# Performance work log

Hardware: AMD Instinct MI355X
Metric: run time of the kernel (lower is better)

Reference implementation:

```python
import jax, jax.numpy as jnp
import numpy as np

G = 128          # occupancy/feature grid resolution (hardcoded in module)
S = 128          # marching steps per ray (max_steps)
N_RAYS = 262144  # 512x512 image
AABB_MIN = jnp.array([-1.0, -0.5, -1.0], dtype=jnp.float32)
AABB_MAX = jnp.array([ 1.0,  0.5,  1.0], dtype=jnp.float32)
MIN_NEAR = 0.05
DENSITY_THRESH = 0.01
T_THRESH = 1e-4


def setup_inputs() -> dict:
    key = jax.random.key(0)
    k1, k2, k3, k4, k5 = jax.random.split(key, 5)
    rays_o = jnp.array([0.0, 0.0, 2.5], dtype=jnp.float32) + 0.1 * jax.random.normal(k1, (N_RAYS, 3), dtype=jnp.float32)
    target = AABB_MIN + (AABB_MAX - AABB_MIN) * jax.random.uniform(k2, (N_RAYS, 3), dtype=jnp.float32)
    d = target - rays_o
    rays_d = d / jnp.linalg.norm(d, axis=-1, keepdims=True)
    sigma_grid = jax.random.uniform(k3, (G, G, G), dtype=jnp.float32)
    rgb_grid = jax.random.uniform(k4, (G, G, G, 3), dtype=jnp.float32)
    bg_color = jax.random.uniform(k5, (3,), dtype=jnp.float32)
    return {"rays_o": rays_o, "rays_d": rays_d, "sigma_grid": sigma_grid,
            "rgb_grid": rgb_grid, "bg_color": bg_color}


def _near_far(rays_o, rays_d):
    # slab test against AABB, as in raymarching.near_far_from_aabb
    safe_d = jnp.where(jnp.abs(rays_d) < 1e-9, 1e-9, rays_d)
    t1 = (AABB_MIN - rays_o) / safe_d
    t2 = (AABB_MAX - rays_o) / safe_d
    near = jnp.max(jnp.minimum(t1, t2), axis=-1)
    far = jnp.min(jnp.maximum(t1, t2), axis=-1)
    near = jnp.maximum(near, MIN_NEAR)
    far = jnp.maximum(far, near + 1e-6)
    return near, far


def _trilerp(sigma_grid, rgb_grid, pos):
    # pos: [N,3] world coords -> grid coords in [0, G-1]
    u = (pos - AABB_MIN) / (AABB_MAX - AABB_MIN) * (G - 1)
    u = jnp.clip(u, 0.0, G - 1.0)
    u0 = jnp.clip(jnp.floor(u), 0.0, G - 2.0)
    f = u - u0                              # [N,3] fractional weights
    u0 = u0.astype(jnp.int32)
    sig = jnp.zeros(pos.shape[0], dtype=pos.dtype)
    rgb = jnp.zeros((pos.shape[0], 3), dtype=pos.dtype)
    for dx in (0, 1):
        wx = f[:, 0] if dx else (1.0 - f[:, 0])
        ix = u0[:, 0] + dx
        for dy in (0, 1):
            wy = f[:, 1] if dy else (1.0 - f[:, 1])
            iy = u0[:, 1] + dy
            for dz in (0, 1):
                wz = f[:, 2] if dz else (1.0 - f[:, 2])
                iz = u0[:, 2] + dz
                w = wx * wy * wz
                sig = sig + w * sigma_grid[ix, iy, iz]
                rgb = rgb + w[:, None] * rgb_grid[ix, iy, iz]
    return sig, rgb


def _render(rays_o, rays_d, sigma_grid, rgb_grid, bg_color):
    near, far = _near_far(rays_o, rays_d)
    dt = (far - near) / S                    # per-ray step size

    def step(carry, i):
        T, ws, depth, image = carry
        t = near + (i + 0.5) * dt            # [N] sample depth
        pos = rays_o + t[:, None] * rays_d   # [N,3]
        sig, rgb = _trilerp(sigma_grid, rgb_grid, pos)
        # occupancy-grid empty-space skip: zero density below threshold
        sig = jnp.where(sig > DENSITY_THRESH, sig, 0.0)
        alpha = 1.0 - jnp.exp(-sig * dt)
        # early ray termination (T_thresh) as in composite_rays
        alpha = jnp.where(T > T_THRESH, alpha, 0.0)
        w = alpha * T
        return (T * (1.0 - alpha), ws + w, depth + w * t,
                image + w[:, None] * rgb), None

    N = rays_o.shape[0]
    init = (jnp.ones(N, jnp.float32), jnp.zeros(N, jnp.float32),
            jnp.zeros(N, jnp.float32), jnp.zeros((N, 3), jnp.float32))
    (T, ws, depth, image), _ = jax.lax.scan(step, init,
                                            jnp.arange(S, dtype=jnp.float32))
    image = jnp.clip(image + (1.0 - ws)[:, None] * bg_color, 0.0, 1.0)
    depth = jnp.clip(depth - near, 0.0, None) / (far - near)
    return image, depth, ws


def reference(rays_o, rays_d, sigma_grid, rgb_grid, bg_color):
    image, depth, weights_sum = _render(rays_o, rays_d, sigma_grid, rgb_grid, bg_color)
    return image
```

## Files before the change

kernel.cpp:

```cpp
#include <hip/hip_runtime.h>


constexpr int   kG     = 128;
constexpr int   kG3    = kG * kG * kG;
constexpr int   kSteps = 128;
constexpr int   kNRays = 262144;
constexpr int   kKB    = 1 << 22;
constexpr float kBminX = -1.0f, kBminY = -0.5f, kBminZ = -1.0f;
constexpr float kBmaxX =  1.0f, kBmaxY =  0.5f, kBmaxZ =  1.0f;
constexpr float kSx = 63.5f, kSy = 127.0f, kSz = 63.5f;
constexpr float kMinNear = 0.05f;
constexpr float kTTh     = 1e-4f;

#if __has_builtin(__builtin_amdgcn_udot4)
#define USE_UDOT4 1
constexpr float kScale  = 65025.0f;
#else
#define USE_UDOT4 0
constexpr float kScale  = 255.0f;
#endif
constexpr float kInvScale = 1.0f / kScale;
constexpr float kSigThr   = 0.01f * kScale;

__device__ __forceinline__ void slabNearFar(
    float ox, float oy, float oz, float dx, float dy, float dz,
    float& near_, float& far_)
{
    float sdx = (fabsf(dx) < 1e-9f) ? 1e-9f : dx;
    float sdy = (fabsf(dy) < 1e-9f) ? 1e-9f : dy;
    float sdz = (fabsf(dz) < 1e-9f) ? 1e-9f : dz;
    float t1x = (kBminX - ox) / sdx, t2x = (kBmaxX - ox) / sdx;
    float t1y = (kBminY - oy) / sdy, t2y = (kBmaxY - oy) / sdy;
    float t1z = (kBminZ - oz) / sdz, t2z = (kBmaxZ - oz) / sdz;
    near_ = fmaxf(fmaxf(fminf(t1x, t2x), fminf(t1y, t2y)), fminf(t1z, t2z));
    far_  = fminf(fminf(fmaxf(t1x, t2x), fmaxf(t1y, t2y)), fmaxf(t1z, t2z));
    near_ = fmaxf(near_, kMinNear);
    far_  = fmaxf(far_, near_ + 1e-6f);
}

__device__ __forceinline__ void cellOf(
    float u0x, float u0y, float u0z, float dux, float duy, float duz,
    float sf, int& cell, float& fx, float& fy, float& fz)
{
    float ux = fminf(fmaxf(fmaf(sf, dux, u0x), 0.0f), 127.0f);
    float uy = fminf(fmaxf(fmaf(sf, duy, u0y), 0.0f), 127.0f);
    float uz = fminf(fmaxf(fmaf(sf, duz, u0z), 0.0f), 127.0f);
    float cx = fminf(floorf(ux), 126.0f);
    float cy = fminf(floorf(uy), 126.0f);
    float cz = fminf(floorf(uz), 126.0f);
    fx = ux - cx; fy = uy - cy; fz = uz - cz;
    cell = ((int)cy << 14) + ((int)cz << 7) + (int)cx;
}

__device__ __forceinline__ int pathKey22(
    float ox, float oy, float oz, float dx, float dy, float dz,
    float near_, float far_)
{
    float exw = fmaf(near_, dx, ox), eyw = fmaf(near_, dy, oy);
    int ex = min(31, max(0, (int)((exw - kBminX) * 16.0f)));
    int ey = min(31, max(0, (int)((eyw - kBminY) * 32.0f)));
    float xx = fmaf(far_, dx, ox), xy = fmaf(far_, dy, oy), xz = fmaf(far_, dz, oz);
    int qx = min(15, max(0, (int)((xx - kBminX) * 8.0f)));
    int qy = min(15, max(0, (int)((xy - kBminY) * 16.0f)));
    int qz = min(15, max(0, (int)((xz - kBminZ) * 8.0f)));
    return (((ey << 5) | ex) << 12) | (qx << 8) | (qy << 4) | qz;
}

__device__ __forceinline__ unsigned packvox8(
    const float* __restrict__ sig, const float* __restrict__ rgb, int idx)
{
    unsigned s = (unsigned)__float2int_rn(fminf(fmaxf(sig[idx], 0.f), 1.f) * 255.f);
    unsigned r = (unsigned)__float2int_rn(fminf(fmaxf(rgb[3*idx+0], 0.f), 1.f) * 255.f);
    unsigned g = (unsigned)__float2int_rn(fminf(fmaxf(rgb[3*idx+1], 0.f), 1.f) * 255.f);
    unsigned b = (unsigned)__float2int_rn(fminf(fmaxf(rgb[3*idx+2], 0.f), 1.f) * 255.f);
    return s | (r << 8) | (g << 16) | (b << 24);
}

__global__ __launch_bounds__(128) void fat_k(
    const float* __restrict__ sig, const float* __restrict__ rgb,
    uint4* __restrict__ gout,
    const float* __restrict__ rays_o, const float* __restrict__ rays_d,
    int* __restrict__ hist)
{
    int bid = blockIdx.x;
    if (bid < kG * kG) {
        __shared__ unsigned row[2][kG];
        int ix  = bid >> 7;
        int iy0 = bid & 127;
        int iy1 = min(iy0 + 1, 127);
        int z   = threadIdx.x;
        row[0][z] = packvox8(sig, rgb, (ix << 14) + (iy0 << 7) + z);
        row[1][z] = packvox8(sig, rgb, (ix << 14) + (iy1 << 7) + z);
        __syncthreads();
        int z1 = min(z + 1, 127);
        unsigned a = row[0][z], b = row[0][z1], c = row[1][z], d = row[1][z1];
        uint4 cell;
        cell.x = ( a        & 0xffu)        | (( b        & 0xffu) << 8)
               | ((c        & 0xffu) << 16) | (( d        & 0xffu) << 24);
        cell.y = ((a >>  8) & 0xffu)        | (((b >>  8) & 0xffu) << 8)
               | (((c >> 8) & 0xffu) << 16) | (((d >>  8) & 0xffu) << 24);
        cell.z = ((a >> 16) & 0xffu)        | (((b >> 16) & 0xffu) << 8)
               | (((c >> 16) & 0xffu) << 16)| (((d >> 16) & 0xffu) << 24);
        cell.w = ( a >> 24)                 | (( b >> 24) << 8)
               | ((c >> 24) << 16)          | (( d >> 24) << 24);
        gout[(iy0 << 14) + (z << 7) + ix] = cell;
    } else {
        int i = (bid - kG * kG) * 128 + (int)threadIdx.x;
        if (i >= kNRays) return;
        float ox = rays_o[3*i+0], oy = rays_o[3*i+1], oz = rays_o[3*i+2];
        float dx = rays_d[3*i+0], dy = rays_d[3*i+1], dz = rays_d[3*i+2];
        float near_, far_;
        slabNearFar(ox, oy, oz, dx, dy, dz, near_, far_);
        atomicAdd(&hist[pathKey22(ox, oy, oz, dx, dy, dz, near_, far_)], 1);
    }
}

__global__ __launch_bounds__(256) void scan_blk_k(
    int* __restrict__ h, int* __restrict__ bsum)
{
    __shared__ int tmp[256];
    int t = threadIdx.x;
    int i = blockIdx.x * 256 + t;
    int v = h[i];
    tmp[t] = v;
    __syncthreads();
    int x = v;
    for (int off = 1; off < 256; off <<= 1) {
        int y = (t >= off) ? tmp[t - off] : 0;
        __syncthreads();
        x += y;
        tmp[t] = x;
        __syncthreads();
    }
    h[i] = x - v;
    if (t == 255) bsum[blockIdx.x] = x;
}

__global__ __launch_bounds__(64) void scan_top64_k(int* __restrict__ b)
{
    int t = threadIdx.x;
    int v = b[t];
    int x = v;
    for (int off = 1; off < 64; off <<= 1) {
        int y = __shfl_up(x, off);
        if (t >= off) x += y;
    }
    b[t] = x - v;
}

__global__ __launch_bounds__(256) void scatter22_k(
    const float* __restrict__ rays_o, const float* __restrict__ rays_d,
    int* __restrict__ h, const int* __restrict__ bsum,
    const int* __restrict__ bsum2, int* __restrict__ perm,
    float4* __restrict__ so4, float4* __restrict__ sd4)
{
    int i = blockIdx.x * 256 + threadIdx.x;
    if (i >= kNRays) return;
    float ox = rays_o[3*i+0], oy = rays_o[3*i+1], oz = rays_o[3*i+2];
    float dx = rays_d[3*i+0], dy = rays_d[3*i+1], dz = rays_d[3*i+2];
    float near_, far_;
    slabNearFar(ox, oy, oz, dx, dy, dz, near_, far_);
    int key = pathKey22(ox, oy, oz, dx, dy, dz, near_, far_);
    float dt = (far_ - near_) * (1.0f / (float)kSteps);
    int pos = bsum2[key >> 16] + bsum[key >> 8] + atomicAdd(&h[key], 1);
    perm[pos] = i;
    so4[pos] = make_float4(ox, oy, oz, near_);
    sd4[pos] = make_float4(dx, dy, dz, dt);
}

__global__ __launch_bounds__(512, 8) void render_f_k(
    const float4* __restrict__ so4, const float4* __restrict__ sd4,
    const uint4* __restrict__ grid, const int* __restrict__ perm,
    const float* __restrict__ bg, float* __restrict__ out)
{
    __shared__ float4 part[256];

    int bid = blockIdx.x;
    int swz = (bid & 7) * 128 + (bid >> 3);
    int t    = (int)threadIdx.x;
    int rloc = t & 255;
    int seg  = t >> 8;
    int sj   = swz * 256 + rloc;

    float4 o4 = so4[sj], d4 = sd4[sj];
    float ox = o4.x, oy = o4.y, oz = o4.z, near_ = o4.w;
    float dx = d4.x, dy = d4.y, dz = d4.z, dt = d4.w;
    float dtq = dt * kInvScale;

    const int nsteps = kSteps / 2;

    float t0  = fmaf(0.5f, dt, near_);
    float u0x = (fmaf(t0, dx, ox) - kBminX) * kSx;
    float u0y = (fmaf(t0, dy, oy) - kBminY) * kSy;
    float u0z = (fmaf(t0, dz, oz) - kBminZ) * kSz;
    float dux = dx * dt * kSx, duy = dy * dt * kSy, duz = dz * dt * kSz;
    float sb = (float)(seg * nsteps);
    u0x = fmaf(sb, dux, u0x); u0y = fmaf(sb, duy, u0y); u0z = fmaf(sb, duz, u0z);

    int c;
    float f0x, f0y, f0z, f1x, f1y, f1z, f2x, f2y, f2z;
    cellOf(u0x, u0y, u0z, dux, duy, duz, 0.0f, c, f0x, f0y, f0z);
    uint4 q0 = grid[c], q1 = grid[c + 1];
    cellOf(u0x, u0y, u0z, dux, duy, duz, 1.0f, c, f1x, f1y, f1z);
    uint4 m0 = grid[c], m1 = grid[c + 1];

    float T = 1.0f, wsum = 0.0f, ar = 0.0f, ag = 0.0f, ab = 0.0f;

    for (int s = 0; s < nsteps; ++s) {
        float sn = (float)min(s + 2, nsteps - 1);
        cellOf(u0x, u0y, u0z, dux, duy, duz, sn, c, f2x, f2y, f2z);
        uint4 n0 = grid[c], n1 = grid[c + 1];

        float wz0 = 1.0f - f0z, wy0 = 1.0f - f0y;
        float sA, sB, rA, rB, gA, gB, bA, bB;
#if USE_UDOT4
        int w00 = __float2int_rn(wy0 * wz0 * 255.0f);
        int w01 = __float2int_rn(wy0 * f0z * 255.0f);
        int w10 = __float2int_rn(f0y * wz0 * 255.0f);
        int w11 = 255 - w00 - w01 - w10;
        w11 = max(w11, 0);
        unsigned wp = (unsigned)(w00 | (w01 << 8) | (w10 << 16) | (w11 << 24));
        sA = (float)__builtin_amdgcn_udot4(q0.x, wp, 0u, false);
        rA = (float)__builtin_amdgcn_udot4(q0.y, wp, 0u, false);
        gA = (float)__builtin_amdgcn_udot4(q0.z, wp, 0u, false);
        bA = (float)__builtin_amdgcn_udot4(q0.w, wp, 0u, false);
        sB = (float)__builtin_amdgcn_udot4(q1.x, wp, 0u, false);
        rB = (float)__builtin_amdgcn_udot4(q1.y, wp, 0u, false);
        gB = (float)__builtin_amdgcn_udot4(q1.z, wp, 0u, false);
        bB = (float)__builtin_amdgcn_udot4(q1.w, wp, 0u, false);
#else
        float w00 = wy0 * wz0, w01 = wy0 * f0z, w10 = f0y * wz0, w11 = f0y * f0z;
        #define CB0(u) ((float)((u) & 0xffu))
        #define CB1(u) ((float)(((u) >> 8) & 0xffu))
        #define CB2(u) ((float)(((u) >> 16) & 0xffu))
        #define CB3(u) ((float)((u) >> 24))
        sA = w00*CB0(q0.x) + w01*CB1(q0.x) + w10*CB2(q0.x) + w11*CB3(q0.x);
        rA = w00*CB0(q0.y) + w01*CB1(q0.y) + w10*CB2(q0.y) + w11*CB3(q0.y);
        gA = w00*CB0(q0.z) + w01*CB1(q0.z) + w10*CB2(q0.z) + w11*CB3(q0.z);
        bA = w00*CB0(q0.w) + w01*CB1(q0.w) + w10*CB2(q0.w) + w11*CB3(q0.w);
        sB = w00*CB0(q1.x) + w01*CB1(q1.x) + w10*CB2(q1.x) + w11*CB3(q1.x);
        rB = w00*CB0(q1.y) + w01*CB1(q1.y) + w10*CB2(q1.y) + w11*CB3(q1.y);
        gB = w00*CB0(q1.z) + w01*CB1(q1.z) + w10*CB2(q1.z) + w11*CB3(q1.z);
        bB = w00*CB0(q1.w) + w01*CB1(q1.w) + w10*CB2(q1.w) + w11*CB3(q1.w);
#endif
        float sv = fmaf(f0x, sB - sA, sA);
        float rv = fmaf(f0x, rB - rA, rA);
        float gv = fmaf(f0x, gB - gA, gA);
        float bv = fmaf(f0x, bB - bA, bA);

        float sigr  = (sv > kSigThr) ? sv : 0.0f;
        float alpha = 1.0f - __expf(-sigr * dtq);
        alpha = (T > kTTh) ? alpha : 0.0f;
        float w = alpha * T;
        T *= (1.0f - alpha);
        wsum += w;
        ar = fmaf(w, rv, ar);
        ag = fmaf(w, gv, ag);
        ab = fmaf(w, bv, ab);

        q0 = m0; q1 = m1; m0 = n0; m1 = n1;
        f0x = f1x; f0y = f1y; f0z = f1z;
        f1x = f2x; f1y = f2y; f1z = f2z;
    }

    if (seg == 1) part[rloc] = make_float4(ar, ag, ab, wsum);
    __syncthreads();
    if (seg == 0) {
        float4 b = part[rloc];
        ar = fmaf(T, b.x, ar);
        ag = fmaf(T, b.y, ag);
        ab = fmaf(T, b.z, ab);
        float ws = fmaf(T, b.w, wsum);
        int ray = perm[sj];
        float omw = 1.0f - ws;
        out[3 * ray + 0] = fminf(fmaxf(fmaf(omw, bg[0], ar * kInvScale), 0.0f), 1.0f);
        out[3 * ray + 1] = fminf(fmaxf(fmaf(omw, bg[1], ag * kInvScale), 0.0f), 1.0f);
        out[3 * ray + 2] = fminf(fmaxf(fmaf(omw, bg[2], ab * kInvScale), 0.0f), 1.0f);
    }
}

__global__ __launch_bounds__(256) void render_plain_k(
    const float* __restrict__ rays_o, const float* __restrict__ rays_d,
    const float* __restrict__ sgrid, const float* __restrict__ cgrid,
    const float* __restrict__ bg, float* __restrict__ out)
{
    int i = blockIdx.x * 256 + threadIdx.x;
    if (i >= kNRays) return;
    float ox = rays_o[3*i+0], oy = rays_o[3*i+1], oz = rays_o[3*i+2];
    float dx = rays_d[3*i+0], dy = rays_d[3*i+1], dz = rays_d[3*i+2];
    float near_, far_;
    slabNearFar(ox, oy, oz, dx, dy, dz, near_, far_);
    float dt = (far_ - near_) * (1.0f / (float)kSteps);
    float t0  = fmaf(0.5f, dt, near_);
    float u0x = (fmaf(t0, dx, ox) - kBminX) * kSx;
    float u0y = (fmaf(t0, dy, oy) - kBminY) * kSy;
    float u0z = (fmaf(t0, dz, oz) - kBminZ) * kSz;
    float dux = dx * dt * kSx, duy = dy * dt * kSy, duz = dz * dt * kSz;
    float T = 1.0f, wsum = 0.0f, accr = 0.0f, accg = 0.0f, accb = 0.0f;
    for (int s = 0; s < kSteps; ++s) {
        float ux = fminf(fmaxf(fmaf((float)s, dux, u0x), 0.0f), 127.0f);
        float uy = fminf(fmaxf(fmaf((float)s, duy, u0y), 0.0f), 127.0f);
        float uz = fminf(fmaxf(fmaf((float)s, duz, u0z), 0.0f), 127.0f);
        float cx = fminf(floorf(ux), 126.0f);
        float cy = fminf(floorf(uy), 126.0f);
        float cz = fminf(floorf(uz), 126.0f);
        float fx = ux - cx, fy = uy - cy, fz = uz - cz;
        int base = ((int)cx << 14) + ((int)cy << 7) + (int)cz;
        float w0x = 1.0f - fx, w0y = 1.0f - fy, w0z = 1.0f - fz;
        float wa = w0x*w0y*w0z, wb = w0x*w0y*fz, wc = w0x*fy*w0z, wd = w0x*fy*fz;
        float we = fx*w0y*w0z,  wf = fx*w0y*fz,  wg = fx*fy*w0z,  wh = fx*fy*fz;
        int i000 = base, i001 = base + 1, i010 = base + kG, i011 = base + kG + 1;
        int i100 = base + kG*kG, i101 = i100 + 1, i110 = i100 + kG, i111 = i110 + 1;
        float sv = wa*sgrid[i000] + wb*sgrid[i001] + wc*sgrid[i010] + wd*sgrid[i011]
                 + we*sgrid[i100] + wf*sgrid[i101] + wg*sgrid[i110] + wh*sgrid[i111];
        float rv = wa*cgrid[3*i000+0] + wb*cgrid[3*i001+0] + wc*cgrid[3*i010+0] + wd*cgrid[3*i011+0]
                 + we*cgrid[3*i100+0] + wf*cgrid[3*i101+0] + wg*cgrid[3*i110+0] + wh*cgrid[3*i111+0];
        float gv = wa*cgrid[3*i000+1] + wb*cgrid[3*i001+1] + wc*cgrid[3*i010+1] + wd*cgrid[3*i011+1]
                 + we*cgrid[3*i100+1] + wf*cgrid[3*i101+1] + wg*cgrid[3*i110+1] + wh*cgrid[3*i111+1];
        float bv = wa*cgrid[3*i000+2] + wb*cgrid[3*i001+2] + wc*cgrid[3*i010+2] + wd*cgrid[3*i011+2]
                 + we*cgrid[3*i100+2] + wf*cgrid[3*i101+2] + wg*cgrid[3*i110+2] + wh*cgrid[3*i111+2];
        float sig = (sv > 0.01f) ? sv : 0.0f;
        float alpha = 1.0f - __expf(-sig * dt);
        float w = alpha * T;
        T *= (1.0f - alpha);
        wsum += w;
        accr = fmaf(w, rv, accr); accg = fmaf(w, gv, accg); accb = fmaf(w, bv, accb);
        if (T <= kTTh) break;
    }
    float omw = 1.0f - wsum;
    out[3 * i + 0] = fminf(fmaxf(fmaf(omw, bg[0], accr), 0.0f), 1.0f);
    out[3 * i + 1] = fminf(fmaxf(fmaf(omw, bg[1], accg), 0.0f), 1.0f);
    out[3 * i + 2] = fminf(fmaxf(fmaf(omw, bg[2], accb), 0.0f), 1.0f);
}

extern "C" void kernel_launch(void* const* d_in, const int* in_sizes, int n_in,
                              void* d_out, int out_size, void* d_ws, size_t ws_size,
                              hipStream_t stream)
{
    const float* rays_o = (const float*)d_in[0];
    const float* rays_d = (const float*)d_in[1];
    const float* sgrid  = (const float*)d_in[2];
    const float* cgrid  = (const float*)d_in[3];
    const float* bg     = (const float*)d_in[4];
    float* out = (float*)d_out;

    const int RB_BLK = kNRays / 256;

    size_t a_grid  = 0;
    size_t a_hist  = a_grid  + (size_t)kG3 * sizeof(uint4);
    size_t a_bsum  = a_hist  + (size_t)kKB * sizeof(int);
    size_t a_bsum2 = a_bsum  + (size_t)(kKB / 256) * sizeof(int);
    size_t a_perm  = a_bsum2 + (size_t)64 * sizeof(int);
    size_t a_so4   = a_perm  + (size_t)kNRays * sizeof(int);
    size_t a_sd4   = a_so4   + (size_t)kNRays * sizeof(float4);
    size_t needA   = a_sd4   + (size_t)kNRays * sizeof(float4);

    if (ws_size >= needA) {
        char* ws = (char*)d_ws;
        uint4*  grid  = (uint4*)(ws + a_grid);
        int*    hist  = (int*)(ws + a_hist);
        int*    bsum  = (int*)(ws + a_bsum);
        int*    bsum2 = (int*)(ws + a_bsum2);
        int*    perm  = (int*)(ws + a_perm);
        float4* so4   = (float4*)(ws + a_so4);
        float4* sd4   = (float4*)(ws + a_sd4);

        hipMemsetAsync(hist, 0, (size_t)kKB * sizeof(int), stream);
        fat_k<<<kG * kG + kNRays / 128, 128, 0, stream>>>(
            sgrid, cgrid, grid, rays_o, rays_d, hist);
        scan_blk_k<<<kKB / 256, 256, 0, stream>>>(hist, bsum);
        scan_blk_k<<<kKB / 65536, 256, 0, stream>>>(bsum, bsum2);
        scan_top64_k<<<1, 64, 0, stream>>>(bsum2);
        scatter22_k<<<RB_BLK, 256, 0, stream>>>(rays_o, rays_d, hist, bsum,
                                                bsum2, perm, so4, sd4);
        render_f_k<<<kNRays / 256, 512, 0, stream>>>(so4, sd4, grid, perm, bg, out);
    } else {
        render_plain_k<<<RB_BLK, 256, 0, stream>>>(
            rays_o, rays_d, sgrid, cgrid, bg, out);
    }
}
```

Before: 220.8 us.

## Deepen grid prefetch, polynomial alpha, and single-kernel mid-level prefix scan

Extends the software pipeline in the render loop to prefetch grid cells three steps ahead instead of two. Replaces the exp in alpha computation with a cubic Taylor polynomial, valid for small sigma*dt. Merges the second-level and top-level prefix scans into one single-block kernel that carries a running offset, removing a launch and the bsum2 indirection in the scatter. Risks: more registers in the render kernel, a serial single-block scan, and approximation error if sigma*dt becomes large.

```diff
diff --git a/kernel.cpp b/kernel.cpp
--- a/kernel.cpp
+++ b/kernel.cpp
@@ -7,7 +7,6 @@
 constexpr int   kNRays = 262144;
 constexpr int   kKB    = 1 << 22;
 constexpr float kBminX = -1.0f, kBminY = -0.5f, kBminZ = -1.0f;
-constexpr float kBmaxX =  1.0f, kBmaxY =  0.5f, kBmaxZ =  1.0f;
 constexpr float kSx = 63.5f, kSy = 127.0f, kSz = 63.5f;
 constexpr float kMinNear = 0.05f;
 constexpr float kTTh     = 1e-4f;
@@ -29,9 +28,9 @@
     float sdx = (fabsf(dx) < 1e-9f) ? 1e-9f : dx;
     float sdy = (fabsf(dy) < 1e-9f) ? 1e-9f : dy;
     float sdz = (fabsf(dz) < 1e-9f) ? 1e-9f : dz;
-    float t1x = (kBminX - ox) / sdx, t2x = (kBmaxX - ox) / sdx;
-    float t1y = (kBminY - oy) / sdy, t2y = (kBmaxY - oy) / sdy;
-    float t1z = (kBminZ - oz) / sdz, t2z = (kBmaxZ - oz) / sdz;
+    float t1x = (kBminX - ox) / sdx, t2x = (1.0f - ox) / sdx;
+    float t1y = (kBminY - oy) / sdy, t2y = (0.5f - oy) / sdy;
+    float t1z = (kBminZ - oz) / sdz, t2z = (1.0f - oz) / sdz;
     near_ = fmaxf(fmaxf(fminf(t1x, t2x), fminf(t1y, t2y)), fminf(t1z, t2z));
     far_  = fminf(fminf(fmaxf(t1x, t2x), fmaxf(t1y, t2y)), fmaxf(t1z, t2z));
     near_ = fmaxf(near_, kMinNear);
@@ -136,22 +135,36 @@
     if (t == 255) bsum[blockIdx.x] = x;
 }
 
-__global__ __launch_bounds__(64) void scan_top64_k(int* __restrict__ b)
-{
+__global__ __launch_bounds__(256) void scan_mid_k(int* __restrict__ b)
+{
+    __shared__ int tmp[256];
+    __shared__ int carry;
     int t = threadIdx.x;
-    int v = b[t];
-    int x = v;
-    for (int off = 1; off < 64; off <<= 1) {
-        int y = __shfl_up(x, off);
-        if (t >= off) x += y;
-    }
-    b[t] = x - v;
+    if (t == 0) carry = 0;
+    __syncthreads();
+    for (int blk = 0; blk < 64; ++blk) {
+        int i = blk * 256 + t;
+        int v = b[i];
+        tmp[t] = v;
+        __syncthreads();
+        int x = v;
+        for (int off = 1; off < 256; off <<= 1) {
+            int y = (t >= off) ? tmp[t - off] : 0;
+            __syncthreads();
+            x += y;
+            tmp[t] = x;
+            __syncthreads();
+        }
+        b[i] = x - v + carry;
+        __syncthreads();
+        if (t == 255) carry += x;
+        __syncthreads();
+    }
 }
 
 __global__ __launch_bounds__(256) void scatter22_k(
     const float* __restrict__ rays_o, const float* __restrict__ rays_d,
-    int* __restrict__ h, const int* __restrict__ bsum,
-    const int* __restrict__ bsum2, int* __restrict__ perm,
+    int* __restrict__ h, const int* __restrict__ bsum, int* __restrict__ perm,
     float4* __restrict__ so4, float4* __restrict__ sd4)
 {
     int i = blockIdx.x * 256 + threadIdx.x;
@@ -162,7 +175,7 @@
     slabNearFar(ox, oy, oz, dx, dy, dz, near_, far_);
     int key = pathKey22(ox, oy, oz, dx, dy, dz, near_, far_);
     float dt = (far_ - near_) * (1.0f / (float)kSteps);
-    int pos = bsum2[key >> 16] + bsum[key >> 8] + atomicAdd(&h[key], 1);
+    int pos = bsum[key >> 8] + atomicAdd(&h[key], 1);
     perm[pos] = i;
     so4[pos] = make_float4(ox, oy, oz, near_);
     sd4[pos] = make_float4(dx, dy, dz, dt);
@@ -198,18 +211,20 @@
     u0x = fmaf(sb, dux, u0x); u0y = fmaf(sb, duy, u0y); u0z = fmaf(sb, duz, u0z);
 
     int c;
-    float f0x, f0y, f0z, f1x, f1y, f1z, f2x, f2y, f2z;
+    float f0x, f0y, f0z, f1x, f1y, f1z, f2x, f2y, f2z, f3x, f3y, f3z;
     cellOf(u0x, u0y, u0z, dux, duy, duz, 0.0f, c, f0x, f0y, f0z);
     uint4 q0 = grid[c], q1 = grid[c + 1];
     cellOf(u0x, u0y, u0z, dux, duy, duz, 1.0f, c, f1x, f1y, f1z);
     uint4 m0 = grid[c], m1 = grid[c + 1];
+    cellOf(u0x, u0y, u0z, dux, duy, duz, 2.0f, c, f2x, f2y, f2z);
+    uint4 n0 = grid[c], n1 = grid[c + 1];
 
     float T = 1.0f, wsum = 0.0f, ar = 0.0f, ag = 0.0f, ab = 0.0f;
 
     for (int s = 0; s < nsteps; ++s) {
-        float sn = (float)min(s + 2, nsteps - 1);
-        cellOf(u0x, u0y, u0z, dux, duy, duz, sn, c, f2x, f2y, f2z);
-        uint4 n0 = grid[c], n1 = grid[c + 1];
+        float sn = (float)min(s + 3, nsteps - 1);
+        cellOf(u0x, u0y, u0z, dux, duy, duz, sn, c, f3x, f3y, f3z);
+        uint4 p0 = grid[c], p1 = grid[c + 1];
 
         float wz0 = 1.0f - f0z, wy0 = 1.0f - f0y;
         float sA, sB, rA, rB, gA, gB, bA, bB;
@@ -248,8 +263,8 @@
         float gv = fmaf(f0x, gB - gA, gA);
         float bv = fmaf(f0x, bB - bA, bA);
 
-        float sigr  = (sv > kSigThr) ? sv : 0.0f;
-        float alpha = 1.0f - __expf(-sigr * dtq);
+        float x = ((sv > kSigThr) ? sv : 0.0f) * dtq;
+        float alpha = x * fmaf(x, fmaf(x, 0.16666667f, -0.5f), 1.0f);
         alpha = (T > kTTh) ? alpha : 0.0f;
         float w = alpha * T;
         T *= (1.0f - alpha);
@@ -258,9 +273,10 @@
         ag = fmaf(w, gv, ag);
         ab = fmaf(w, bv, ab);
 
-        q0 = m0; q1 = m1; m0 = n0; m1 = n1;
+        q0 = m0; q1 = m1; m0 = n0; m1 = n1; n0 = p0; n1 = p1;
         f0x = f1x; f0y = f1y; f0z = f1z;
         f1x = f2x; f1y = f2y; f1z = f2z;
+        f2x = f3x; f2y = f3y; f2z = f3z;
     }
 
     if (seg == 1) part[rloc] = make_float4(ar, ag, ab, wsum);
@@ -349,8 +365,7 @@
     size_t a_grid  = 0;
     size_t a_hist  = a_grid  + (size_t)kG3 * sizeof(uint4);
     size_t a_bsum  = a_hist  + (size_t)kKB * sizeof(int);
-    size_t a_bsum2 = a_bsum  + (size_t)(kKB / 256) * sizeof(int);
-    size_t a_perm  = a_bsum2 + (size_t)64 * sizeof(int);
+    size_t a_perm  = a_bsum  + (size_t)(kKB / 256) * sizeof(int);
     size_t a_so4   = a_perm  + (size_t)kNRays * sizeof(int);
     size_t a_sd4   = a_so4   + (size_t)kNRays * sizeof(float4);
     size_t needA   = a_sd4   + (size_t)kNRays * sizeof(float4);
@@ -360,7 +375,6 @@
         uint4*  grid  = (uint4*)(ws + a_grid);
         int*    hist  = (int*)(ws + a_hist);
         int*    bsum  = (int*)(ws + a_bsum);
-        int*    bsum2 = (int*)(ws + a_bsum2);
         int*    perm  = (int*)(ws + a_perm);
         float4* so4   = (float4*)(ws + a_so4);
         float4* sd4   = (float4*)(ws + a_sd4);
@@ -369,10 +383,9 @@
         fat_k<<<kG * kG + kNRays / 128, 128, 0, stream>>>(
             sgrid, cgrid, grid, rays_o, rays_d, hist);
         scan_blk_k<<<kKB / 256, 256, 0, stream>>>(hist, bsum);
-        scan_blk_k<<<kKB / 65536, 256, 0, stream>>>(bsum, bsum2);
-        scan_top64_k<<<1, 64, 0, stream>>>(bsum2);
+        scan_mid_k<<<1, 256, 0, stream>>>(bsum);
         scatter22_k<<<RB_BLK, 256, 0, stream>>>(rays_o, rays_d, hist, bsum,
-                                                bsum2, perm, so4, sd4);
+                                                perm, so4, sd4);
         render_f_k<<<kNRays / 256, 512, 0, stream>>>(so4, sd4, grid, perm, bg, out);
     } else {
         render_plain_k<<<RB_BLK, 256, 0, stream>>>(
```

Result: slower. 273.3 us (+23.8%).
